# Performance work log

Hardware: AMD Instinct MI355X
Metric: run time of the kernel (lower is better)

## Reference

```python
import jax, jax.numpy as jnp
import numpy as np

D_MODEL = 1024
NUM_HEADS = 16
HEAD_DIM = D_MODEL // NUM_HEADS


def setup_inputs() -> dict:
    key = jax.random.key(0)
    ks = jax.random.split(key, 11)
    N, S = 4, 2048
    s = 1.0 / np.sqrt(D_MODEL)
    return {
        "query": jax.random.normal(ks[0], (N, S, D_MODEL), jnp.float32),
        "key": jax.random.normal(ks[1], (N, S, D_MODEL), jnp.float32),
        "value": jax.random.normal(ks[2], (N, S, D_MODEL), jnp.float32),
        "Wq": jax.random.normal(ks[3], (D_MODEL, D_MODEL), jnp.float32) * s,
        "bq": jnp.zeros((D_MODEL,), jnp.float32),
        "Wk": jax.random.normal(ks[4], (D_MODEL, D_MODEL), jnp.float32) * s,
        "bk": jnp.zeros((D_MODEL,), jnp.float32),
        "Wv": jax.random.normal(ks[5], (D_MODEL, D_MODEL), jnp.float32) * s,
        "bv": jnp.zeros((D_MODEL,), jnp.float32),
        "Wo": jax.random.normal(ks[6], (D_MODEL, D_MODEL), jnp.float32) * s,
        "bo": jnp.zeros((D_MODEL,), jnp.float32),
    }


def reference(query, key, value, Wq, bq, Wk, bk, Wv, bv, Wo, bo):
    N, Q, _ = query.shape
    K = key.shape[1]
    # torch Linear: x @ W^T + b
    q = (query @ Wq.T + bq).reshape(N, Q, NUM_HEADS, HEAD_DIM)
    k = (key @ Wk.T + bk).reshape(N, K, NUM_HEADS, HEAD_DIM)
    v = (value @ Wv.T + bv).reshape(N, K, NUM_HEADS, HEAD_DIM)
    # NOTE: original module applies NO 1/sqrt(head_dim) scaling.
    scores = jnp.einsum('nqhd,nkhd->nhqk', q, k)
    attn = jax.nn.softmax(scores, axis=3)
    out = jnp.einsum('nhqk,nkhd->nqhd', attn, v).reshape(N, Q, D_MODEL)
    return out @ Wo.T + bo
```

## Files before the change

### kernel.cpp

```cpp
#include <hip/hip_runtime.h>
#include <stdint.h>

#define SEQ 2048
#define MROWS 8192
#define LOG2E 1.44269504f

typedef __attribute__((ext_vector_type(8))) _Float16 f16x8;
typedef __attribute__((ext_vector_type(2))) __fp16 fp16x2_t;
typedef __attribute__((ext_vector_type(8))) unsigned short ushort8;
typedef __attribute__((ext_vector_type(4))) unsigned short ushort4_t;
typedef __attribute__((ext_vector_type(4))) float f32x4;
typedef __attribute__((ext_vector_type(16))) float f32x16;

__device__ __forceinline__ unsigned short f32_to_f16u(float f) {
  union { _Float16 h; unsigned short u; } v; v.h = (_Float16)f; return v.u;
}

__device__ __forceinline__ unsigned int pk_u32(float a, float b) {
  union { fp16x2_t h; unsigned int u; } v;
  v.h = __builtin_amdgcn_cvt_pkrtz(a, b);
  return v.u;
}

__device__ __forceinline__ ushort8 pack8_rtz(float4 f0, float4 f1) {
  union { fp16x2_t h2[4]; ushort8 u8; } pk;
  pk.h2[0] = __builtin_amdgcn_cvt_pkrtz(f0.x, f0.y);
  pk.h2[1] = __builtin_amdgcn_cvt_pkrtz(f0.z, f0.w);
  pk.h2[2] = __builtin_amdgcn_cvt_pkrtz(f1.x, f1.y);
  pk.h2[3] = __builtin_amdgcn_cvt_pkrtz(f1.z, f1.w);
  return pk.u8;
}

__device__ __forceinline__ void gload16(const void* g, void* l) {
  __builtin_amdgcn_global_load_lds(
      (const __attribute__((address_space(1))) unsigned int*)g,
      (__attribute__((address_space(3))) unsigned int*)l, 16, 0, 0);
}

__device__ __forceinline__ void softmax32(f32x16* s, f32x16* o,
                                          float& mrun, float& lrun, f16x8* pf) {
  float m01 = fmaxf(fmaxf(s[0][0], s[0][1]), fmaxf(s[0][2], s[0][3]));
  float m02 = fmaxf(fmaxf(s[0][4], s[0][5]), fmaxf(s[0][6], s[0][7]));
  float m03 = fmaxf(fmaxf(s[0][8], s[0][9]), fmaxf(s[0][10], s[0][11]));
  float m04 = fmaxf(fmaxf(s[0][12], s[0][13]), fmaxf(s[0][14], s[0][15]));
  float m11 = fmaxf(fmaxf(s[1][0], s[1][1]), fmaxf(s[1][2], s[1][3]));
  float m12 = fmaxf(fmaxf(s[1][4], s[1][5]), fmaxf(s[1][6], s[1][7]));
  float m13 = fmaxf(fmaxf(s[1][8], s[1][9]), fmaxf(s[1][10], s[1][11]));
  float m14 = fmaxf(fmaxf(s[1][12], s[1][13]), fmaxf(s[1][14], s[1][15]));
  float ml = fmaxf(fmaxf(fmaxf(m01,m02), fmaxf(m03,m04)),
                   fmaxf(fmaxf(m11,m12), fmaxf(m13,m14)));
  if (!__all(ml <= mrun + 7.0f)) {
    float m2 = fmaxf(ml, __shfl_xor(ml, 32, 64));
    float mn = fmaxf(mrun, m2);
    float sc = __builtin_amdgcn_exp2f(mrun - mn);
    lrun *= sc;
    mrun = mn;
    #pragma unroll
    for (int dd=0; dd<2; ++dd)
      #pragma unroll
      for (int r=0;r<16;++r) o[dd][r] *= sc;
  }
  float m0 = mrun;
  float a0=0.f, a1=0.f, a2=0.f, a3=0.f;
  #pragma unroll
  for (int st=0; st<2; ++st)
    #pragma unroll
    for (int r=0;r<16;r+=4) {
      float p0 = __builtin_amdgcn_exp2f(s[st][r+0] - m0); s[st][r+0] = p0; a0 += p0;
      float p1 = __builtin_amdgcn_exp2f(s[st][r+1] - m0); s[st][r+1] = p1; a1 += p1;
      float p2 = __builtin_amdgcn_exp2f(s[st][r+2] - m0); s[st][r+2] = p2; a2 += p2;
      float p3 = __builtin_amdgcn_exp2f(s[st][r+3] - m0); s[st][r+3] = p3; a3 += p3;
    }
  lrun += (a0 + a1) + (a2 + a3);
  #pragma unroll
  for (int st=0; st<2; ++st)
    #pragma unroll
    for (int s_t=0; s_t<2; ++s_t) {
      unsigned int c0 = pk_u32(s[st][8*s_t+0], s[st][8*s_t+1]);
      unsigned int c1 = pk_u32(s[st][8*s_t+2], s[st][8*s_t+3]);
      unsigned int d0 = pk_u32(s[st][8*s_t+4], s[st][8*s_t+5]);
      unsigned int d1 = pk_u32(s[st][8*s_t+6], s[st][8*s_t+7]);
      asm("v_permlane32_swap_b32 %0, %1" : "+v"(c0), "+v"(d0));
      asm("v_permlane32_swap_b32 %0, %1" : "+v"(c1), "+v"(d1));
      union { unsigned int u[4]; f16x8 v; } pkk;
      pkk.u[0] = c0; pkk.u[1] = c1; pkk.u[2] = d0; pkk.u[3] = d1;
      pf[st*2 + s_t] = pkk.v;
    }
}

__global__ __launch_bounds__(256) void wconv_k(
    const float* __restrict__ Wq, const float* __restrict__ Wk,
    const float* __restrict__ Wv, const float* __restrict__ Wo,
    unsigned short* __restrict__ WF)
{
  const int plane = blockIdx.y;
  const float* __restrict__ s = (plane==0)? Wq : (plane==1)? Wk : (plane==2)? Wv : Wo;
  size_t off = ((size_t)blockIdx.x*256 + threadIdx.x) * 8;
  float4 f0 = *(const float4*)(s + off);
  float4 f1 = *(const float4*)(s + off + 4);
  *(ushort8*)&WF[(size_t)plane*1048576 + off] = pack8_rtz(f0, f1);
}

__global__ __launch_bounds__(256) void qkv_k(
    const float* __restrict__ Aq, const float* __restrict__ Ak, const float* __restrict__ Av,
    const unsigned short* __restrict__ WF,
    const float* __restrict__ bq, const float* __restrict__ bk, const float* __restrict__ bv,
    unsigned short* __restrict__ Qf, unsigned short* __restrict__ Kf, unsigned short* __restrict__ Vt)
{
  const int z = blockIdx.z;
  const float* __restrict__ A    = (z==0)? Aq : (z==1)? Ak : Av;
  const unsigned short* __restrict__ W = WF + (size_t)z*1048576;
  const float* __restrict__ bias = (z==0)? bq : (z==1)? bk : bv;

  __shared__ unsigned short Ah[128*32];
  __shared__ unsigned short Bh[128*32];

  const int tid  = threadIdx.x;
  const int lane = tid & 63;
  const int w    = tid >> 6;
  const int wm   = w >> 1, wn = w & 1;
  const int row0 = blockIdx.x * 128;
  const int col0 = blockIdx.y * 128;

  f32x4 acc[4][4] = {};

  for (int k0 = 0; k0 < 1024; k0 += 32) {
    __syncthreads();
    #pragma unroll
    for (int j=0;j<2;++j) {
      int r  = w*32 + j*16 + (lane>>2);
      int sl = (lane & 3) ^ ((r>>1)&3);
      gload16(W + (size_t)(col0 + r)*1024 + k0 + sl*8, &Bh[(w*32 + j*16)*32]);
    }
    #pragma unroll
    for (int i = 0; i < 2; ++i) {
      int c = tid + i*256;
      int r = c >> 2, slot = c & 3;
      int lidx = r*32 + ((slot ^ ((r >> 1) & 3))*8);
      const float* ap = A + (size_t)(row0 + r)*1024 + k0 + slot*8;
      float4 f0 = *(const float4*)ap;
      float4 f1 = *(const float4*)(ap + 4);
      *(ushort8*)&Ah[lidx] = pack8_rtz(f0, f1);
    }
    __syncthreads();

    f16x8 a_[4], b_[4];
    const int slotR = lane >> 4;
    #pragma unroll
    for (int m=0;m<4;++m) {
      int r = wm*64 + m*16 + (lane & 15);
      a_[m] = *(const f16x8*)&Ah[r*32 + ((slotR ^ ((r>>1)&3))*8)];
    }
    #pragma unroll
    for (int nn=0;nn<4;++nn) {
      int r = wn*64 + nn*16 + (lane & 15);
      b_[nn] = *(const f16x8*)&Bh[r*32 + ((slotR ^ ((r>>1)&3))*8)];
    }
    #pragma unroll
    for (int m=0;m<4;++m)
      #pragma unroll
      for (int nn=0;nn<4;++nn)
        acc[m][nn] = __builtin_amdgcn_mfma_f32_16x16x32_f16(a_[m], b_[nn], acc[m][nn],0,0,0);
  }

  #pragma unroll
  for (int m=0;m<4;++m) {
    #pragma unroll
    for (int nn=0;nn<4;++nn) {
      int gcol = col0 + wn*64 + nn*16 + (lane & 15);
      float bsv = bias[gcol];
      if (z == 2) {
        int rbase = row0 + wm*64 + m*16 + (lane>>4)*4;
        int nIdx = rbase >> 11, s0 = rbase & 2047;
        ushort4_t pk;
        #pragma unroll
        for (int r2=0;r2<4;++r2) pk[r2] = f32_to_f16u(acc[m][nn][r2] + bsv);
        *(ushort4_t*)&Vt[((size_t)(nIdx*1024 + gcol))*2048 + s0] = pk;
      } else {
        unsigned short* __restrict__ dst = (z==0)? Qf : Kf;
        const float qsc = (z==0)? LOG2E : 1.0f;
        #pragma unroll
        for (int r2=0;r2<4;++r2) {
          int grow = row0 + wm*64 + m*16 + (lane>>4)*4 + r2;
          dst[(size_t)grow*1024 + gcol] = f32_to_f16u((acc[m][nn][r2] + bsv) * qsc);
        }
      }
    }
  }
}

__global__ __launch_bounds__(256) void oproj_k(
    const unsigned short* __restrict__ AO, const unsigned short* __restrict__ W,
    const float* __restrict__ bias, float* __restrict__ out)
{
  __shared__ unsigned short Ah[128*32];
  __shared__ unsigned short Bh[128*32];

  const int tid  = threadIdx.x;
  const int lane = tid & 63;
  const int w    = tid >> 6;
  const int wm   = w >> 1, wn = w & 1;
  const int row0 = blockIdx.x * 128;
  const int col0 = blockIdx.y * 128;

  f32x4 acc[4][4] = {};

  for (int k0 = 0; k0 < 1024; k0 += 32) {
    __syncthreads();
    #pragma unroll
    for (int j=0;j<2;++j) {
      int r  = w*32 + j*16 + (lane>>2);
      int sl = (lane & 3) ^ ((r>>1)&3);
      gload16(AO + (size_t)(row0 + r)*1024 + k0 + sl*8, &Ah[(w*32 + j*16)*32]);
      gload16(W  + (size_t)(col0 + r)*1024 + k0 + sl*8, &Bh[(w*32 + j*16)*32]);
    }
    __syncthreads();

    f16x8 a_[4], b_[4];
    const int slotR = lane >> 4;
    #pragma unroll
    for (int m=0;m<4;++m) {
      int r = wm*64 + m*16 + (lane & 15);
      a_[m] = *(const f16x8*)&Ah[r*32 + ((slotR ^ ((r>>1)&3))*8)];
    }
    #pragma unroll
    for (int nn=0;nn<4;++nn) {
      int r = wn*64 + nn*16 + (lane & 15);
      b_[nn] = *(const f16x8*)&Bh[r*32 + ((slotR ^ ((r>>1)&3))*8)];
    }
    #pragma unroll
    for (int m=0;m<4;++m)
      #pragma unroll
      for (int nn=0;nn<4;++nn)
        acc[m][nn] = __builtin_amdgcn_mfma_f32_16x16x32_f16(a_[m], b_[nn], acc[m][nn],0,0,0);
  }

  #pragma unroll
  for (int m=0;m<4;++m)
    #pragma unroll
    for (int nn=0;nn<4;++nn) {
      int gcol = col0 + wn*64 + nn*16 + (lane & 15);
      float bsv = bias[gcol];
      #pragma unroll
      for (int r2=0;r2<4;++r2) {
        int grow = row0 + wm*64 + m*16 + (lane>>4)*4 + r2;
        out[(size_t)grow*1024 + gcol] = acc[m][nn][r2] + bsv;
      }
    }
}

__global__ __launch_bounds__(512) void attn_k(
  const unsigned short* __restrict__ Qf, const unsigned short* __restrict__ Kf,
  const unsigned short* __restrict__ Vt, unsigned short* __restrict__ AO)
{
  __shared__ unsigned short Ks[2][64*64];
  __shared__ unsigned short Vs[2][64*64];

  const int tid = threadIdx.x, lane = tid & 63, w = tid >> 6;
  const int q = lane & 31, h = lane >> 5;

  const int bid = blockIdx.x;
  const int swz = (bid & 7) * 64 + (bid >> 3);
  const int qt = swz & 7, nh = swz >> 3;
  const int n = nh >> 4, hh = nh & 15;

  f16x8 qf[4];
  {
    int qrow = n*SEQ + qt*256 + w*32 + q;
    #pragma unroll
    for (int t=0;t<4;++t)
      qf[t] = *(const f16x8*)&Qf[(size_t)qrow*1024 + hh*64 + t*16 + h*8];
  }

  f32x16 o[2] = {};
  float mrun = -1e30f, lrun = 0.f;

  const size_t kbase = (size_t)(n*SEQ)*1024 + hh*64;
  const size_t vbase = ((size_t)(n*1024 + hh*64))*SEQ;

  const int sr = tid >> 3, ssl = tid & 7;
  const int slidx = sr*64 + ((ssl^(sr&7))*8);

  const unsigned short* kp = Kf + kbase + (size_t)sr*1024 + ssl*8;
  const unsigned short* vp = Vt + vbase + (size_t)sr*SEQ  + ssl*8;

  *(ushort8*)&Ks[0][slidx] = *(const ushort8*)kp;
  *(ushort8*)&Vs[0][slidx] = *(const ushort8*)vp;
  ushort8 kregA = *(const ushort8*)(kp + 65536);
  ushort8 vregA = *(const ushort8*)(vp + 64);
  kp += 2*65536; vp += 128;
  __syncthreads();

  int cur = 0;
  for (int kt = 0; kt < 32; ++kt) {
    ushort8 kregB, vregB;
    if (kt + 2 < 32) {
      kregB = *(const ushort8*)kp;
      vregB = *(const ushort8*)vp;
      kp += 65536; vp += 64;
    }

    f32x16 s[2] = {};
    __builtin_amdgcn_s_setprio(1);
    #pragma unroll
    for (int t=0; t<4; ++t) {
      int gr = ((2*t+h) ^ (q&7))*8;
      f16x8 k0 = *(const f16x8*)&Ks[cur][(q     )*64 + gr];
      f16x8 k1 = *(const f16x8*)&Ks[cur][(32 + q)*64 + gr];
      s[0] = __builtin_amdgcn_mfma_f32_32x32x16_f16(k0, qf[t], s[0],0,0,0);
      s[1] = __builtin_amdgcn_mfma_f32_32x32x16_f16(k1, qf[t], s[1],0,0,0);
    }
    __builtin_amdgcn_s_setprio(0);

    f16x8 pf[4];
    softmax32(s, o, mrun, lrun, pf);

    __builtin_amdgcn_s_setprio(1);
    #pragma unroll
    for (int sg=0; sg<4; ++sg) {
      int gr = ((2*sg+h) ^ (q&7))*8;
      f16x8 v0 = *(const f16x8*)&Vs[cur][(q     )*64 + gr];
      f16x8 v1 = *(const f16x8*)&Vs[cur][(32 + q)*64 + gr];
      o[0] = __builtin_amdgcn_mfma_f32_32x32x16_f16(v0, pf[sg], o[0],0,0,0);
      o[1] = __builtin_amdgcn_mfma_f32_32x32x16_f16(v1, pf[sg], o[1],0,0,0);
    }
    __builtin_amdgcn_s_setprio(0);

    if (kt + 1 < 32) {
      *(ushort8*)&Ks[cur^1][slidx] = kregA;
      *(ushort8*)&Vs[cur^1][slidx] = vregA;
    }
    __syncthreads();
    kregA = kregB; vregA = vregB;
    cur ^= 1;
  }

  float rs = lrun + __shfl_xor(lrun, 32, 64);
  float inv = 1.0f / rs;
  int qrow = n*SEQ + qt*256 + w*32 + q;
  #pragma unroll
  for (int dd=0; dd<2; ++dd)
    #pragma unroll
    for (int rq=0; rq<4; ++rq) {
      union { fp16x2_t h2[2]; ushort4_t u4; } pk4;
      pk4.h2[0] = __builtin_amdgcn_cvt_pkrtz(o[dd][4*rq+0]*inv, o[dd][4*rq+1]*inv);
      pk4.h2[1] = __builtin_amdgcn_cvt_pkrtz(o[dd][4*rq+2]*inv, o[dd][4*rq+3]*inv);
      int d0 = dd*32 + 8*rq + 4*h;
      *(ushort4_t*)&AO[(size_t)qrow*1024 + hh*64 + d0] = pk4.u4;
    }
}

extern "C" void kernel_launch(void* const* d_in, const int* in_sizes, int n_in,
                              void* d_out, int out_size, void* d_ws, size_t ws_size,
                              hipStream_t stream)
{
  (void)in_sizes; (void)n_in; (void)out_size; (void)ws_size;
  const float* query = (const float*)d_in[0];
  const float* key   = (const float*)d_in[1];
  const float* value = (const float*)d_in[2];
  const float* Wq = (const float*)d_in[3];
  const float* bq = (const float*)d_in[4];
  const float* Wk = (const float*)d_in[5];
  const float* bk = (const float*)d_in[6];
  const float* Wv = (const float*)d_in[7];
  const float* bv = (const float*)d_in[8];
  const float* Wo = (const float*)d_in[9];
  const float* bo = (const float*)d_in[10];
  float* out = (float*)d_out;

  unsigned short* ws = (unsigned short*)d_ws;
  const size_t PLANE = (size_t)MROWS * 1024;
  unsigned short* Qf = ws;
  unsigned short* Kf = Qf + PLANE;
  unsigned short* Vt = Kf + PLANE;
  unsigned short* AO = Vt + PLANE;
  unsigned short* WF = AO + PLANE;

  dim3 bb(256);
  wconv_k<<<dim3(512,4),  bb, 0, stream>>>(Wq, Wk, Wv, Wo, WF);
  qkv_k <<<dim3(64,8,3),  bb, 0, stream>>>(query, key, value, WF, bq, bk, bv, Qf, Kf, Vt);
  attn_k<<<dim3(512), dim3(512), 0, stream>>>(Qf, Kf, Vt, AO);
  oproj_k<<<dim3(64,8),   bb, 0, stream>>>(AO, WF + 3*1048576, bo, out);
}
```

Before: 208.0 us.

## Double-buffer LDS tiles and prefetch next K-slab in QKV and output projections

Both projection GEMMs now use two LDS buffers per operand. The next K-slab is issued as direct global-to-LDS loads while MFMAs run on the current one, and the QKV kernel also keeps fp32 activation data in registers two steps ahead, converting it to fp16 after compute. This drops one barrier per iteration and hides global load latency. MFMA sections are wrapped in s_setprio to favour the issuing wave. LDS use and register pressure both double, which may lower occupancy.

```diff
diff --git a/kernel.cpp b/kernel.cpp
--- a/kernel.cpp
+++ b/kernel.cpp
@@ -112,8 +112,8 @@
   const unsigned short* __restrict__ W = WF + (size_t)z*1048576;
   const float* __restrict__ bias = (z==0)? bq : (z==1)? bk : bv;
 
-  __shared__ unsigned short Ah[128*32];
-  __shared__ unsigned short Bh[128*32];
+  __shared__ unsigned short Ah[2][128*32];
+  __shared__ unsigned short Bh[2][128*32];
 
   const int tid  = threadIdx.x;
   const int lane = tid & 63;
@@ -122,45 +122,85 @@
   const int row0 = blockIdx.x * 128;
   const int col0 = blockIdx.y * 128;
 
+  const float* aptr[2]; int alidx[2];
+  #pragma unroll
+  for (int i=0;i<2;++i) {
+    int c = tid + i*256;
+    int r = c >> 2, slot = c & 3;
+    alidx[i] = r*32 + ((slot ^ ((r>>1)&3))*8);
+    aptr[i]  = A + (size_t)(row0 + r)*1024 + slot*8;
+  }
+
   f32x4 acc[4][4] = {};
 
-  for (int k0 = 0; k0 < 1024; k0 += 32) {
-    __syncthreads();
-    #pragma unroll
-    for (int j=0;j<2;++j) {
-      int r  = w*32 + j*16 + (lane>>2);
-      int sl = (lane & 3) ^ ((r>>1)&3);
-      gload16(W + (size_t)(col0 + r)*1024 + k0 + sl*8, &Bh[(w*32 + j*16)*32]);
-    }
-    #pragma unroll
-    for (int i = 0; i < 2; ++i) {
-      int c = tid + i*256;
-      int r = c >> 2, slot = c & 3;
-      int lidx = r*32 + ((slot ^ ((r >> 1) & 3))*8);
-      const float* ap = A + (size_t)(row0 + r)*1024 + k0 + slot*8;
-      float4 f0 = *(const float4*)ap;
-      float4 f1 = *(const float4*)(ap + 4);
-      *(ushort8*)&Ah[lidx] = pack8_rtz(f0, f1);
-    }
-    __syncthreads();
+  #pragma unroll
+  for (int j=0;j<2;++j) {
+    int r  = w*32 + j*16 + (lane>>2);
+    int sl = (lane & 3) ^ ((r>>1)&3);
+    gload16(W + (size_t)(col0 + r)*1024 + sl*8, &Bh[0][(w*32 + j*16)*32]);
+  }
+  #pragma unroll
+  for (int i=0;i<2;++i) {
+    float4 f0 = *(const float4*)(aptr[i]);
+    float4 f1 = *(const float4*)(aptr[i] + 4);
+    *(ushort8*)&Ah[0][alidx[i]] = pack8_rtz(f0, f1);
+  }
+  float4 ra[2][2];
+  #pragma unroll
+  for (int i=0;i<2;++i) {
+    ra[i][0] = *(const float4*)(aptr[i] + 32);
+    ra[i][1] = *(const float4*)(aptr[i] + 36);
+  }
+  __syncthreads();
+
+  for (int kk = 0; kk < 32; ++kk) {
+    const int cur = kk & 1;
+    if (kk < 31) {
+      #pragma unroll
+      for (int j=0;j<2;++j) {
+        int r  = w*32 + j*16 + (lane>>2);
+        int sl = (lane & 3) ^ ((r>>1)&3);
+        gload16(W + (size_t)(col0 + r)*1024 + (kk+1)*32 + sl*8,
+                &Bh[cur^1][(w*32 + j*16)*32]);
+      }
+    }
+    float4 na[2][2];
+    if (kk < 30) {
+      #pragma unroll
+      for (int i=0;i<2;++i) {
+        na[i][0] = *(const float4*)(aptr[i] + (kk+2)*32);
+        na[i][1] = *(const float4*)(aptr[i] + (kk+2)*32 + 4);
+      }
+    }
 
     f16x8 a_[4], b_[4];
     const int slotR = lane >> 4;
     #pragma unroll
     for (int m=0;m<4;++m) {
       int r = wm*64 + m*16 + (lane & 15);
-      a_[m] = *(const f16x8*)&Ah[r*32 + ((slotR ^ ((r>>1)&3))*8)];
+      a_[m] = *(const f16x8*)&Ah[cur][r*32 + ((slotR ^ ((r>>1)&3))*8)];
     }
     #pragma unroll
     for (int nn=0;nn<4;++nn) {
       int r = wn*64 + nn*16 + (lane & 15);
-      b_[nn] = *(const f16x8*)&Bh[r*32 + ((slotR ^ ((r>>1)&3))*8)];
-    }
+      b_[nn] = *(const f16x8*)&Bh[cur][r*32 + ((slotR ^ ((r>>1)&3))*8)];
+    }
+    __builtin_amdgcn_s_setprio(1);
     #pragma unroll
     for (int m=0;m<4;++m)
       #pragma unroll
       for (int nn=0;nn<4;++nn)
         acc[m][nn] = __builtin_amdgcn_mfma_f32_16x16x32_f16(a_[m], b_[nn], acc[m][nn],0,0,0);
+    __builtin_amdgcn_s_setprio(0);
+
+    if (kk < 31) {
+      #pragma unroll
+      for (int i=0;i<2;++i)
+        *(ushort8*)&Ah[cur^1][alidx[i]] = pack8_rtz(ra[i][0], ra[i][1]);
+    }
+    __syncthreads();
+    #pragma unroll
+    for (int i=0;i<2;++i) { ra[i][0] = na[i][0]; ra[i][1] = na[i][1]; }
   }
 
   #pragma unroll
@@ -193,8 +233,8 @@
     const unsigned short* __restrict__ AO, const unsigned short* __restrict__ W,
     const float* __restrict__ bias, float* __restrict__ out)
 {
-  __shared__ unsigned short Ah[128*32];
-  __shared__ unsigned short Bh[128*32];
+  __shared__ unsigned short Ah[2][128*32];
+  __shared__ unsigned short Bh[2][128*32];
 
   const int tid  = threadIdx.x;
   const int lane = tid & 63;
@@ -205,34 +245,47 @@
 
   f32x4 acc[4][4] = {};
 
-  for (int k0 = 0; k0 < 1024; k0 += 32) {
-    __syncthreads();
-    #pragma unroll
-    for (int j=0;j<2;++j) {
-      int r  = w*32 + j*16 + (lane>>2);
-      int sl = (lane & 3) ^ ((r>>1)&3);
-      gload16(AO + (size_t)(row0 + r)*1024 + k0 + sl*8, &Ah[(w*32 + j*16)*32]);
-      gload16(W  + (size_t)(col0 + r)*1024 + k0 + sl*8, &Bh[(w*32 + j*16)*32]);
-    }
-    __syncthreads();
+  #pragma unroll
+  for (int j=0;j<2;++j) {
+    int r  = w*32 + j*16 + (lane>>2);
+    int sl = (lane & 3) ^ ((r>>1)&3);
+    gload16(AO + (size_t)(row0 + r)*1024 + sl*8, &Ah[0][(w*32 + j*16)*32]);
+    gload16(W  + (size_t)(col0 + r)*1024 + sl*8, &Bh[0][(w*32 + j*16)*32]);
+  }
+  __syncthreads();
+
+  for (int kk = 0; kk < 32; ++kk) {
+    const int cur = kk & 1;
+    if (kk < 31) {
+      #pragma unroll
+      for (int j=0;j<2;++j) {
+        int r  = w*32 + j*16 + (lane>>2);
+        int sl = (lane & 3) ^ ((r>>1)&3);
+        gload16(AO + (size_t)(row0 + r)*1024 + (kk+1)*32 + sl*8, &Ah[cur^1][(w*32 + j*16)*32]);
+        gload16(W  + (size_t)(col0 + r)*1024 + (kk+1)*32 + sl*8, &Bh[cur^1][(w*32 + j*16)*32]);
+      }
+    }
 
     f16x8 a_[4], b_[4];
     const int slotR = lane >> 4;
     #pragma unroll
     for (int m=0;m<4;++m) {
       int r = wm*64 + m*16 + (lane & 15);
-      a_[m] = *(const f16x8*)&Ah[r*32 + ((slotR ^ ((r>>1)&3))*8)];
+      a_[m] = *(const f16x8*)&Ah[cur][r*32 + ((slotR ^ ((r>>1)&3))*8)];
     }
     #pragma unroll
     for (int nn=0;nn<4;++nn) {
       int r = wn*64 + nn*16 + (lane & 15);
-      b_[nn] = *(const f16x8*)&Bh[r*32 + ((slotR ^ ((r>>1)&3))*8)];
-    }
+      b_[nn] = *(const f16x8*)&Bh[cur][r*32 + ((slotR ^ ((r>>1)&3))*8)];
+    }
+    __builtin_amdgcn_s_setprio(1);
     #pragma unroll
     for (int m=0;m<4;++m)
       #pragma unroll
       for (int nn=0;nn<4;++nn)
         acc[m][nn] = __builtin_amdgcn_mfma_f32_16x16x32_f16(a_[m], b_[nn], acc[m][nn],0,0,0);
+    __builtin_amdgcn_s_setprio(0);
+    __syncthreads();
   }
 
   #pragma unroll
```

After: 225.2 us. 8.3% more time.
